# Kernel optimization log

Hardware: AMD Instinct MI355X
Metric: run time of the kernel (lower is better)

The kernel has to match this reference:

```python
import math
import jax, jax.numpy as jnp
import numpy as np

DIM = 1024
NUM_HEADS = 16
HEAD_DIM = DIM // NUM_HEADS


def setup_inputs() -> dict:
    key = jax.random.key(0)
    ks = jax.random.split(key, 5)
    b, t, d = 2, 2048, DIM
    x = jax.random.normal(ks[0], (b, t, d), dtype=jnp.float32)
    mask = jnp.ones((b, t), dtype=jnp.float32)  # 1 = keep, 0 = pad
    s_in = 1.0 / math.sqrt(d)
    w_qkv = jax.random.normal(ks[1], (3 * d, d), dtype=jnp.float32) * s_in
    b_qkv = jnp.zeros((3 * d,), dtype=jnp.float32)
    w_out = jax.random.normal(ks[2], (d, d), dtype=jnp.float32) * s_in
    b_out = jnp.zeros((d,), dtype=jnp.float32)
    return {"x": x, "mask": mask, "w_qkv": w_qkv, "b_qkv": b_qkv,
            "w_out": w_out, "b_out": b_out}


def reference(x, mask, w_qkv, b_qkv, w_out, b_out):
    b, t, d = x.shape
    h, hd = NUM_HEADS, HEAD_DIM
    # qkv projection (torch Linear: x @ W^T + b)
    qkv = x @ w_qkv.T + b_qkv                          # [b,t,3d]
    q, k, v = jnp.split(qkv, 3, axis=-1)
    def reshape(z):
        return z.reshape(b, t, h, hd).transpose(0, 2, 1, 3)  # [b,h,t,hd]
    q, k, v = reshape(q), reshape(k), reshape(v)
    att = jnp.einsum('bhqd,bhkd->bhqk', q, k) / math.sqrt(hd)  # [b,h,t,t]
    causal = jnp.tril(jnp.ones((t, t), dtype=bool))            # [t,t]
    keep = causal[None, None, :, :] & (mask[:, None, None, :] != 0)
    att = jnp.where(keep, att, -jnp.inf)
    att = jax.nn.softmax(att, axis=-1)
    out = jnp.einsum('bhqk,bhkd->bhqd', att, v)        # [b,h,t,hd]
    out = out.transpose(0, 2, 1, 3).reshape(b, t, d)
    return out @ w_out.T + b_out
```

## Files before the change

kernel.cpp:

```cpp
#include <hip/hip_runtime.h>
#include <cmath>

#define B_ 2
#define T_ 2048
#define D_ 1024
#define H_ 16
#define HD_ 64
#define M_ (B_ * T_)
#define N3_ (3 * D_)
#define K_ 1024

typedef _Float16 halfx8 __attribute__((ext_vector_type(8)));
typedef _Float16 halfx4 __attribute__((ext_vector_type(4)));
typedef _Float16 halfx2 __attribute__((ext_vector_type(2)));
typedef __fp16 fp16x2 __attribute__((ext_vector_type(2)));
typedef float f32x4 __attribute__((ext_vector_type(4)));
typedef float f32x16 __attribute__((ext_vector_type(16)));

#define ASYNC_COPY16(gp, lp) \
  __builtin_amdgcn_global_load_lds((__attribute__((address_space(1))) void*)(gp), \
      (__attribute__((address_space(3))) void*)(lp), 16, 0, 0)

#define QSCALE 0.1803368801111204f
#define RTHR 4.0f

__device__ __forceinline__ float exp2fast(float x) {
#if __has_builtin(__builtin_amdgcn_exp2f)
    return __builtin_amdgcn_exp2f(x);
#else
    return exp2f(x);
#endif
}

__device__ const int QT_OF[72] = {
    15,15,15,15,15,15,15,15, 14,14,14,14,14,14,14,14,
    13,13,13,13,13,13,13, 12,12,12,12,12,12,12,
    11,11,11,11,11,11, 10,10,10,10,10,10,
    9,9,9,9,9, 8,8,8,8,8, 7,7,7,7, 6,6,6,6,
    5,5,5, 4,4,4, 3,3, 2,2, 1, 0};
__device__ const int C_OF[72] = {
    0,1,2,3,4,5,6,7, 0,1,2,3,4,5,6,7,
    0,1,2,3,4,5,6, 0,1,2,3,4,5,6,
    0,1,2,3,4,5, 0,1,2,3,4,5,
    0,1,2,3,4, 0,1,2,3,4, 0,1,2,3, 0,1,2,3,
    0,1,2, 0,1,2, 0,1, 0,1, 0, 0};
__device__ const int CB_OF[16] = {0,1,2,4,6,9,12,16,20,25,30,36,42,49,56,64};
__device__ const int NC_OF[16] = {1,1,2,2,3,3,4,4,5,5,6,6,7,7,8,8};
#define NSLOT 72
#define NPOSLOT 56

__global__ __launch_bounds__(256) void prep_all(
    const float* __restrict__ x, const float* __restrict__ wq,
    const float* __restrict__ wo, const float* __restrict__ mask,
    _Float16* __restrict__ xh, _Float16* __restrict__ wqh,
    _Float16* __restrict__ woh, float* __restrict__ kbias,
    int* __restrict__ tflags)
{
    int bid = blockIdx.x;
    if (bid >= 4096) {
        int i = (bid - 4096) * 256 + threadIdx.x;
        float mv = mask[i];
        kbias[i] = (mv != 0.f) ? 0.f : -INFINITY;
        unsigned long long bal = __ballot(mv != 0.f);
        if ((threadIdx.x & 63) == 0) tflags[i >> 6] = (bal == ~0ULL) ? 1 : 0;
        return;
    }
    const float* s; _Float16* d; int off;
    if (bid < 2048)      { s = x;  d = xh;  off = bid; }
    else if (bid < 3584) { s = wq; d = wqh; off = bid - 2048; }
    else                 { s = wo; d = woh; off = bid - 3584; }
    int i = (off * 256 + threadIdx.x) * 8;
    float4 a = *(const float4*)(s + i);
    float4 b = *(const float4*)(s + i + 4);
    halfx8 h;
    h[0] = (_Float16)a.x; h[1] = (_Float16)a.y; h[2] = (_Float16)a.z; h[3] = (_Float16)a.w;
    h[4] = (_Float16)b.x; h[5] = (_Float16)b.y; h[6] = (_Float16)b.z; h[7] = (_Float16)b.w;
    *(halfx8*)(d + i) = h;
}

__global__ __launch_bounds__(256) void gemm_qkv(
    const _Float16* __restrict__ A, const _Float16* __restrict__ Wt,
    const float* __restrict__ bias,
    _Float16* __restrict__ qh, _Float16* __restrict__ kh, _Float16* __restrict__ vth)
{
    __shared__ _Float16 As[128 * 32];
    __shared__ _Float16 Bs[128 * 32];
    const int tid = threadIdx.x;
    const int lane = tid & 63, w = tid >> 6;
    const int col = lane & 15, quad = lane >> 4;
    const int wr = w >> 1, wc = w & 1;
    const int m0 = blockIdx.y << 7, n0 = blockIdx.x << 7;

    const int c0 = w * 2, c1 = c0 + 1;
    const int r0 = c0 * 16 + (lane >> 2), r1 = c1 * 16 + (lane >> 2);
    const int ks = (lane & 3) << 3;

    f32x4 acc[4][4] = {};

    for (int k0 = 0; k0 < K_; k0 += 32) {
        ASYNC_COPY16(A  + (size_t)(m0 + r0) * K_ + k0 + ks, &As[c0 * 512]);
        ASYNC_COPY16(A  + (size_t)(m0 + r1) * K_ + k0 + ks, &As[c1 * 512]);
        ASYNC_COPY16(Wt + (size_t)(n0 + r0) * K_ + k0 + ks, &Bs[c0 * 512]);
        ASYNC_COPY16(Wt + (size_t)(n0 + r1) * K_ + k0 + ks, &Bs[c1 * 512]);
        __syncthreads();
        halfx8 af[4], bf[4];
#pragma unroll
        for (int i = 0; i < 4; ++i)
            af[i] = *(const halfx8*)&As[(wr * 64 + i * 16 + col) * 32 + quad * 8];
#pragma unroll
        for (int j = 0; j < 4; ++j)
            bf[j] = *(const halfx8*)&Bs[(wc * 64 + j * 16 + col) * 32 + quad * 8];
#pragma unroll
        for (int i = 0; i < 4; ++i)
#pragma unroll
            for (int j = 0; j < 4; ++j)
                acc[i][j] = __builtin_amdgcn_mfma_f32_16x16x32_f16(af[i], bf[j], acc[i][j], 0, 0, 0);
        __syncthreads();
    }

#pragma unroll
    for (int i = 0; i < 4; ++i) {
#pragma unroll
        for (int r = 0; r < 4; ++r) {
            int m = m0 + wr * 64 + i * 16 + quad * 4 + r;
            int bb = m >> 11, tt = m & (T_ - 1);
#pragma unroll
            for (int j = 0; j < 4; ++j) {
                int n = n0 + wc * 64 + j * 16 + col;
                float val = acc[i][j][r] + bias[n];
                int which = n >> 10, head = (n >> 6) & 15, dd = n & 63;
                if (which == 0) {
                    qh[((size_t)(bb * H_ + head) * T_ + tt) * HD_ + dd] = (_Float16)(val * QSCALE);
                } else if (which == 1) {
                    int hi = ((dd >> 3) ^ (tt & 7) ^ ((tt >> 3) & 7)) & 7;
                    int dds = (hi << 3) | (dd & 7);
                    kh[((size_t)(bb * H_ + head) * T_ + tt) * HD_ + dds] = (_Float16)val;
                } else {
                    int hi = (((tt >> 3) & 7) ^ (dd & 7) ^ ((dd >> 3) & 7)) & 7;
                    int tts = (tt & ~63) | (hi << 3) | (tt & 7);
                    vth[((size_t)(bb * H_ + head) * HD_ + dd) * T_ + tts] = (_Float16)val;
                }
            }
        }
    }
}

__global__ __launch_bounds__(256) void gemm_out(
    const _Float16* __restrict__ A, const _Float16* __restrict__ Wt,
    const float* __restrict__ bias, float* __restrict__ C)
{
    __shared__ _Float16 As[128 * 32];
    __shared__ _Float16 Bs[64 * 32];
    const int tid = threadIdx.x;
    const int lane = tid & 63, w = tid >> 6;
    const int col = lane & 15, quad = lane >> 4;
    const int m0 = blockIdx.y << 7, n0 = blockIdx.x << 6;

    const int c0 = w * 2, c1 = c0 + 1;
    const int rA0 = c0 * 16 + (lane >> 2), rA1 = c1 * 16 + (lane >> 2);
    const int rB = w * 16 + (lane >> 2);
    const int ks = (lane & 3) << 3;

    f32x4 acc[2][4] = {};

    for (int k0 = 0; k0 < K_; k0 += 32) {
        ASYNC_COPY16(A  + (size_t)(m0 + rA0) * K_ + k0 + ks, &As[c0 * 512]);
        ASYNC_COPY16(A  + (size_t)(m0 + rA1) * K_ + k0 + ks, &As[c1 * 512]);
        ASYNC_COPY16(Wt + (size_t)(n0 + rB) * K_ + k0 + ks, &Bs[w * 512]);
        __syncthreads();
        halfx8 af[2], bf[4];
#pragma unroll
        for (int i = 0; i < 2; ++i)
            af[i] = *(const halfx8*)&As[(w * 32 + i * 16 + col) * 32 + quad * 8];
#pragma unroll
        for (int j = 0; j < 4; ++j)
            bf[j] = *(const halfx8*)&Bs[(j * 16 + col) * 32 + quad * 8];
#pragma unroll
        for (int i = 0; i < 2; ++i)
#pragma unroll
            for (int j = 0; j < 4; ++j)
                acc[i][j] = __builtin_amdgcn_mfma_f32_16x16x32_f16(af[i], bf[j], acc[i][j], 0, 0, 0);
        __syncthreads();
    }

#pragma unroll
    for (int i = 0; i < 2; ++i) {
#pragma unroll
        for (int r = 0; r < 4; ++r) {
            int m = m0 + w * 32 + i * 16 + quad * 4 + r;
#pragma unroll
            for (int j = 0; j < 4; ++j) {
                int n = n0 + j * 16 + col;
                C[(size_t)m * D_ + n] = acc[i][j][r] + bias[n];
            }
        }
    }
}

__global__ __launch_bounds__(256, 3) void attn_kernel(
    const _Float16* __restrict__ qh, const _Float16* __restrict__ kh,
    const _Float16* __restrict__ vth, const float* __restrict__ kbias,
    const int* __restrict__ tflags,
    float* __restrict__ pm, float* __restrict__ pl,
    _Float16* __restrict__ po, _Float16* __restrict__ oh)
{
    __shared__ _Float16 Ks[2][64 * 64];
    __shared__ _Float16 Vt[2][64 * 64];

    const int xi = blockIdx.x;
    const int qt = QT_OF[xi], c = C_OF[xi];
    const int h = blockIdx.y, b = blockIdx.z;
    const int tid = threadIdx.x;
    const int lane = tid & 63, w = tid >> 6;
    const int l31 = lane & 31, q2 = lane >> 5;

    const int kt0 = c * 4;
    const int ktend = min(2 * qt + 1, kt0 + 3);

    const int bh = b * H_ + h;
    const _Float16* qp = qh + (size_t)bh * T_ * HD_;
    const _Float16* kp = kh + (size_t)bh * T_ * HD_;
    const _Float16* vp = vth + (size_t)bh * HD_ * T_;
    const float* kb = kbias + (size_t)b * T_;
    const int* tf = tflags + b * 32;

    const int qbase = qt * 128 + w * 32;
    const int q_row = qbase + l31;

    halfx8 bq[4];
#pragma unroll
    for (int hc = 0; hc < 4; ++hc)
        bq[hc] = *(const halfx8*)(qp + (size_t)q_row * HD_ + hc * 16 + q2 * 8);

    float mrow = -INFINITY;
    float lrow = 0.f;
    f32x16 oacc[2] = {};
    const fp16x2 one2 = {(__fp16)1.f, (__fp16)1.f};

    {
        const _Float16* ksrc = kp + (size_t)(kt0 * 64 + w * 16) * HD_;
        ASYNC_COPY16(ksrc + lane * 8, &Ks[0][(w * 16) * 64]);
        ASYNC_COPY16(ksrc + 8 * HD_ + lane * 8, &Ks[0][(w * 16 + 8) * 64]);
        const _Float16* vsrc = vp + (size_t)(w * 16 + (lane >> 3)) * T_
                                 + kt0 * 64 + (lane & 7) * 8;
        ASYNC_COPY16(vsrc, &Vt[0][(w * 16) * 64]);
        ASYNC_COPY16(vsrc + 8 * T_, &Vt[0][(w * 16 + 8) * 64]);
    }

    for (int kt = kt0; kt <= ktend; ++kt) {
        const int cur = (kt - kt0) & 1;
        __syncthreads();
        if (kt < ktend) {
            const int nb = cur ^ 1;
            const _Float16* ksrc = kp + (size_t)((kt + 1) * 64 + w * 16) * HD_;
            ASYNC_COPY16(ksrc + lane * 8, &Ks[nb][(w * 16) * 64]);
            ASYNC_COPY16(ksrc + 8 * HD_ + lane * 8, &Ks[nb][(w * 16 + 8) * 64]);
            const _Float16* vsrc = vp + (size_t)(w * 16 + (lane >> 3)) * T_
                                     + (kt + 1) * 64 + (lane & 7) * 8;
            ASYNC_COPY16(vsrc, &Vt[nb][(w * 16) * 64]);
            ASYNC_COPY16(vsrc + 8 * T_, &Vt[nb][(w * 16 + 8) * 64]);
        }
        if (kt * 64 > qbase + 31) continue;

        const int allkeep = tf[kt];
        const int kb2max = (qbase + 31 - kt * 64 >= 32) ? 2 : 1;

        auto qk_half = [&](int kb2v) -> f32x16 {
            f32x16 a = {};
#pragma unroll
            for (int hc = 0; hc < 4; ++hc) {
                int seg = (hc * 2 + q2) ^ (l31 & 7) ^ ((kb2v * 4 + (l31 >> 3)) & 7);
                halfx8 ka = *(const halfx8*)&Ks[cur][(kb2v * 32 + l31) * 64 + seg * 8];
                a = __builtin_amdgcn_mfma_f32_32x32x16_f16(ka, bq[hc], a, 0, 0, 0);
            }
            return a;
        };
        f32x16 sa0, sa1;
        __builtin_amdgcn_s_setprio(1);
        sa0 = qk_half(0);
        if (kb2max == 2) sa1 = qk_half(1);
        __builtin_amdgcn_s_setprio(0);

        auto smpv = [&](const f32x16& a, int kb2v) {
            float t0 = fmaxf(fmaxf(a[0],  a[1]),  a[2]);
            float t1 = fmaxf(fmaxf(a[3],  a[4]),  a[5]);
            float t2 = fmaxf(fmaxf(a[6],  a[7]),  a[8]);
            float t3 = fmaxf(fmaxf(a[9],  a[10]), a[11]);
            float t4 = fmaxf(fmaxf(a[12], a[13]), a[14]);
            float u0 = fmaxf(fmaxf(t0, t1), t2);
            float u1 = fmaxf(fmaxf(t3, t4), a[15]);
            float mx = fmaxf(u0, u1);

            if (__any(mx > mrow + RTHR)) {
                float mxo = fmaxf(mx, __shfl_xor(mx, 32, 64));
                float mnew = fmaxf(mrow, mxo);
                float alpha = exp2fast(mrow - mnew);
                lrow *= alpha;
#pragma unroll
                for (int db = 0; db < 2; ++db)
#pragma unroll
                    for (int r = 0; r < 16; ++r) oacc[db][r] *= alpha;
                mrow = mnew;
            }

            const bool fastk = allkeep && (kt * 64 + kb2v * 32 + 31 <= qbase);
            halfx4 pf[4];
            float s0 = 0.f, s1 = 0.f;
            if (fastk) {
#pragma unroll
                for (int cc = 0; cc < 4; ++cc) {
                    float e0 = exp2fast(a[cc * 4 + 0] - mrow);
                    float e1 = exp2fast(a[cc * 4 + 1] - mrow);
                    float e2 = exp2fast(a[cc * 4 + 2] - mrow);
                    float e3 = exp2fast(a[cc * 4 + 3] - mrow);
                    fp16x2 lo = __builtin_amdgcn_cvt_pkrtz(e0, e1);
                    fp16x2 hi = __builtin_amdgcn_cvt_pkrtz(e2, e3);
                    halfx2* pfv = (halfx2*)&pf[cc];
                    pfv[0] = __builtin_bit_cast(halfx2, lo);
                    pfv[1] = __builtin_bit_cast(halfx2, hi);
#if __has_builtin(__builtin_amdgcn_fdot2)
                    s0 = __builtin_amdgcn_fdot2(lo, one2, s0, false);
                    s1 = __builtin_amdgcn_fdot2(hi, one2, s1, false);
#else
                    s0 += e0 + e1; s1 += e2 + e3;
#endif
                }
            } else {
#pragma unroll
                for (int cc = 0; cc < 4; ++cc) {
                    float e[4];
#pragma unroll
                    for (int j = 0; j < 4; ++j) {
                        int key = kt * 64 + kb2v * 32 + 8 * cc + 4 * q2 + j;
                        float add = allkeep ? 0.f : kb[key];
                        e[j] = (key <= q_row) ? exp2fast(a[cc * 4 + j] + add - mrow) : 0.f;
                    }
                    fp16x2 lo = __builtin_amdgcn_cvt_pkrtz(e[0], e[1]);
                    fp16x2 hi = __builtin_amdgcn_cvt_pkrtz(e[2], e[3]);
                    halfx2* pfv = (halfx2*)&pf[cc];
                    pfv[0] = __builtin_bit_cast(halfx2, lo);
                    pfv[1] = __builtin_bit_cast(halfx2, hi);
#if __has_builtin(__builtin_amdgcn_fdot2)
                    s0 = __builtin_amdgcn_fdot2(lo, one2, s0, false);
                    s1 = __builtin_amdgcn_fdot2(hi, one2, s1, false);
#else
                    s0 += e[0] + e[1]; s1 += e[2] + e[3];
#endif
                }
            }
            lrow += s0 + s1;

            __builtin_amdgcn_s_setprio(1);
#pragma unroll
            for (int db = 0; db < 2; ++db)
#pragma unroll
                for (int cc = 0; cc < 4; ++cc) {
                    int ck = kb2v * 4 + cc;
                    int seg = ck ^ (l31 & 7) ^ ((db * 4 + (l31 >> 3)) & 7);
                    halfx4 va = *(const halfx4*)&Vt[cur][(db * 32 + l31) * 64 + seg * 8 + q2 * 4];
                    oacc[db] = __builtin_amdgcn_mfma_f32_32x32x8f16(va, pf[cc], oacc[db], 0, 0, 0);
                }
            __builtin_amdgcn_s_setprio(0);
        };

        smpv(sa0, 0);
        if (kb2max == 2) smpv(sa1, 1);
    }

    lrow += __shfl_xor(lrow, 32, 64);

    const int qloc = w * 32 + l31;
    const int slot = bh * NSLOT + CB_OF[qt] + c;
    if (q2 == 0) {
        pm[(size_t)slot * 128 + qloc] = mrow;
        pl[(size_t)slot * 128 + qloc] = lrow;
    }
    _Float16* pob;
    if (c == 0)
        pob = oh + ((size_t)(b * T_ + qt * 128 + qloc)) * D_ + h * 64;
    else
        pob = po + ((size_t)(bh * NPOSLOT + (CB_OF[qt] - qt) + (c - 1)) * 128 + qloc) * 64;
#pragma unroll
    for (int db = 0; db < 2; ++db)
#pragma unroll
        for (int gg = 0; gg < 4; ++gg) {
            halfx4 ov;
#pragma unroll
            for (int j = 0; j < 4; ++j)
                ov[j] = (_Float16)(oacc[db][gg * 4 + j]);
            *(halfx4*)(pob + db * 32 + 8 * gg + 4 * q2) = ov;
        }
}

__global__ __launch_bounds__(256) void attn_combine(
    const float* __restrict__ pm, const float* __restrict__ pl,
    const _Float16* __restrict__ po, _Float16* __restrict__ oh)
{
    const int qt = blockIdx.x, h = blockIdx.y, b = blockIdx.z;
    const int nc = NC_OF[qt], cb = CB_OF[qt];
    const int bh = b * H_ + h;
    const int tid = threadIdx.x;
    const int r = tid >> 1, dh = tid & 1;

    const int slot0 = bh * NSLOT + cb;
    float mc[8], lc[8];
    float mstar = -INFINITY;
    for (int cc = 0; cc < nc; ++cc) {
        mc[cc] = pm[(size_t)(slot0 + cc) * 128 + r];
        lc[cc] = pl[(size_t)(slot0 + cc) * 128 + r];
        mstar = fmaxf(mstar, mc[cc]);
    }
    float lstar = 0.f, wc[8];
    for (int cc = 0; cc < nc; ++cc) {
        wc[cc] = exp2f(mc[cc] - mstar);
        lstar += wc[cc] * lc[cc];
    }

    _Float16* ohrow = oh + ((size_t)(b * T_ + qt * 128 + r)) * D_ + h * 64 + dh * 32;

    float acc[32];
    {
        float wv = wc[0];
#pragma unroll
        for (int g = 0; g < 4; ++g) {
            halfx8 hv = *(const halfx8*)(ohrow + g * 8);
#pragma unroll
            for (int j = 0; j < 8; ++j)
                acc[g * 8 + j] = wv * (float)hv[j];
        }
    }
    const int pbase = bh * NPOSLOT + (cb - qt);
    for (int cc = 1; cc < nc; ++cc) {
        const _Float16* src = po + ((size_t)(pbase + cc - 1) * 128 + r) * 64 + dh * 32;
        float wv = wc[cc];
#pragma unroll
        for (int g = 0; g < 4; ++g) {
            halfx8 hv = *(const halfx8*)(src + g * 8);
#pragma unroll
            for (int j = 0; j < 8; ++j)
                acc[g * 8 + j] += wv * (float)hv[j];
        }
    }
    float linv = 1.f / lstar;
#pragma unroll
    for (int g = 0; g < 4; ++g) {
        halfx8 ov;
#pragma unroll
        for (int j = 0; j < 8; ++j)
            ov[j] = (_Float16)(acc[g * 8 + j] * linv);
        *(halfx8*)(ohrow + g * 8) = ov;
    }
}

extern "C" void kernel_launch(void* const* d_in, const int* in_sizes, int n_in,
                              void* d_out, int out_size, void* d_ws, size_t ws_size,
                              hipStream_t stream)
{
    (void)in_sizes; (void)n_in; (void)out_size; (void)ws_size;
    const float* x     = (const float*)d_in[0];
    const float* mask  = (const float*)d_in[1];
    const float* w_qkv = (const float*)d_in[2];
    const float* b_qkv = (const float*)d_in[3];
    const float* w_out = (const float*)d_in[4];
    const float* b_out = (const float*)d_in[5];
    float* out = (float*)d_out;

    const size_t QKV1 = (size_t)B_ * H_ * T_ * HD_;
    _Float16* xh  = (_Float16*)d_ws;
    _Float16* wqh = xh  + (size_t)M_ * K_;
    _Float16* woh = wqh + (size_t)N3_ * K_;
    _Float16* qh  = woh + (size_t)D_ * K_;
    _Float16* kh  = qh  + QKV1;
    _Float16* vth = kh  + QKV1;
    _Float16* oh  = vth + QKV1;
    _Float16* po  = oh  + QKV1;
    float* kbias  = (float*)(po + (size_t)32 * NPOSLOT * 128 * 64);
    float* pm     = kbias + (size_t)B_ * T_;
    float* pl     = pm + (size_t)32 * NSLOT * 128;
    int* tflags   = (int*)(pl + (size_t)32 * NSLOT * 128);

    prep_all<<<4112, 256, 0, stream>>>(x, w_qkv, w_out, mask,
                                       xh, wqh, woh, kbias, tflags);
    gemm_qkv<<<dim3(N3_ / 128, M_ / 128), 256, 0, stream>>>(
        xh, wqh, b_qkv, qh, kh, vth);
    attn_kernel<<<dim3(72, H_, B_), 256, 0, stream>>>(
        qh, kh, vth, kbias, tflags, pm, pl, po, oh);
    attn_combine<<<dim3(16, H_, B_), 256, 0, stream>>>(
        pm, pl, po, oh);
    gemm_out<<<dim3(D_ / 64, M_ / 128), 256, 0, stream>>>(
        oh, woh, b_out, out);
}
```

Measured before the change: 196.8 us.

## Drop split-K attention chunks and combine kernel; one block per query tile

Attention blocks now each process a full 128-row query tile against all causal key tiles, launched as a flat 512-block grid ordered from longest to shortest. The partial max/sum/output buffers and the separate combine kernel are removed, and normalization by the row sum happens in the epilogue. This removes a launch and partial-result memory traffic, but it reduces the number of blocks and lengthens the critical path of the largest query tiles, which risks underfilling the GPU.

```diff
diff --git a/kernel.cpp b/kernel.cpp
--- a/kernel.cpp
+++ b/kernel.cpp
@@ -31,23 +31,6 @@
     return exp2f(x);
 #endif
 }
-
-__device__ const int QT_OF[72] = {
-    15,15,15,15,15,15,15,15, 14,14,14,14,14,14,14,14,
-    13,13,13,13,13,13,13, 12,12,12,12,12,12,12,
-    11,11,11,11,11,11, 10,10,10,10,10,10,
-    9,9,9,9,9, 8,8,8,8,8, 7,7,7,7, 6,6,6,6,
-    5,5,5, 4,4,4, 3,3, 2,2, 1, 0};
-__device__ const int C_OF[72] = {
-    0,1,2,3,4,5,6,7, 0,1,2,3,4,5,6,7,
-    0,1,2,3,4,5,6, 0,1,2,3,4,5,6,
-    0,1,2,3,4,5, 0,1,2,3,4,5,
-    0,1,2,3,4, 0,1,2,3,4, 0,1,2,3, 0,1,2,3,
-    0,1,2, 0,1,2, 0,1, 0,1, 0, 0};
-__device__ const int CB_OF[16] = {0,1,2,4,6,9,12,16,20,25,30,36,42,49,56,64};
-__device__ const int NC_OF[16] = {1,1,2,2,3,3,4,4,5,5,6,6,7,7,8,8};
-#define NSLOT 72
-#define NPOSLOT 56
 
 __global__ __launch_bounds__(256) void prep_all(
     const float* __restrict__ x, const float* __restrict__ wq,
@@ -201,21 +184,21 @@
     const _Float16* __restrict__ qh, const _Float16* __restrict__ kh,
     const _Float16* __restrict__ vth, const float* __restrict__ kbias,
     const int* __restrict__ tflags,
-    float* __restrict__ pm, float* __restrict__ pl,
-    _Float16* __restrict__ po, _Float16* __restrict__ oh)
+    _Float16* __restrict__ oh)
 {
     __shared__ _Float16 Ks[2][64 * 64];
     __shared__ _Float16 Vt[2][64 * 64];
 
-    const int xi = blockIdx.x;
-    const int qt = QT_OF[xi], c = C_OF[xi];
-    const int h = blockIdx.y, b = blockIdx.z;
+    const int bid = blockIdx.x;
+    const int qt = 15 - (bid >> 5);
+    const int hb = bid & 31;
+    const int h = hb & 15, b = hb >> 4;
     const int tid = threadIdx.x;
     const int lane = tid & 63, w = tid >> 6;
     const int l31 = lane & 31, q2 = lane >> 5;
 
-    const int kt0 = c * 4;
-    const int ktend = min(2 * qt + 1, kt0 + 3);
+    const int kt0 = 0;
+    const int ktend = 2 * qt + 1;
 
     const int bh = b * H_ + h;
     const _Float16* qp = qh + (size_t)bh * T_ * HD_;
@@ -368,18 +351,10 @@
     }
 
     lrow += __shfl_xor(lrow, 32, 64);
+    const float linv = 1.f / lrow;
 
     const int qloc = w * 32 + l31;
-    const int slot = bh * NSLOT + CB_OF[qt] + c;
-    if (q2 == 0) {
-        pm[(size_t)slot * 128 + qloc] = mrow;
-        pl[(size_t)slot * 128 + qloc] = lrow;
-    }
-    _Float16* pob;
-    if (c == 0)
-        pob = oh + ((size_t)(b * T_ + qt * 128 + qloc)) * D_ + h * 64;
-    else
-        pob = po + ((size_t)(bh * NPOSLOT + (CB_OF[qt] - qt) + (c - 1)) * 128 + qloc) * 64;
+    _Float16* pob = oh + ((size_t)(b * T_ + qt * 128 + qloc)) * D_ + h * 64;
 #pragma unroll
     for (int db = 0; db < 2; ++db)
 #pragma unroll
@@ -387,69 +362,9 @@
             halfx4 ov;
 #pragma unroll
             for (int j = 0; j < 4; ++j)
-                ov[j] = (_Float16)(oacc[db][gg * 4 + j]);
+                ov[j] = (_Float16)(oacc[db][gg * 4 + j] * linv);
             *(halfx4*)(pob + db * 32 + 8 * gg + 4 * q2) = ov;
         }
-}
-
-__global__ __launch_bounds__(256) void attn_combine(
-    const float* __restrict__ pm, const float* __restrict__ pl,
-    const _Float16* __restrict__ po, _Float16* __restrict__ oh)
-{
-    const int qt = blockIdx.x, h = blockIdx.y, b = blockIdx.z;
-    const int nc = NC_OF[qt], cb = CB_OF[qt];
-    const int bh = b * H_ + h;
-    const int tid = threadIdx.x;
-    const int r = tid >> 1, dh = tid & 1;
-
-    const int slot0 = bh * NSLOT + cb;
-    float mc[8], lc[8];
-    float mstar = -INFINITY;
-    for (int cc = 0; cc < nc; ++cc) {
-        mc[cc] = pm[(size_t)(slot0 + cc) * 128 + r];
-        lc[cc] = pl[(size_t)(slot0 + cc) * 128 + r];
-        mstar = fmaxf(mstar, mc[cc]);
-    }
-    float lstar = 0.f, wc[8];
-    for (int cc = 0; cc < nc; ++cc) {
-        wc[cc] = exp2f(mc[cc] - mstar);
-        lstar += wc[cc] * lc[cc];
-    }
-
-    _Float16* ohrow = oh + ((size_t)(b * T_ + qt * 128 + r)) * D_ + h * 64 + dh * 32;
-
-    float acc[32];
-    {
-        float wv = wc[0];
-#pragma unroll
-        for (int g = 0; g < 4; ++g) {
-            halfx8 hv = *(const halfx8*)(ohrow + g * 8);
-#pragma unroll
-            for (int j = 0; j < 8; ++j)
-                acc[g * 8 + j] = wv * (float)hv[j];
-        }
-    }
-    const int pbase = bh * NPOSLOT + (cb - qt);
-    for (int cc = 1; cc < nc; ++cc) {
-        const _Float16* src = po + ((size_t)(pbase + cc - 1) * 128 + r) * 64 + dh * 32;
-        float wv = wc[cc];
-#pragma unroll
-        for (int g = 0; g < 4; ++g) {
-            halfx8 hv = *(const halfx8*)(src + g * 8);
-#pragma unroll
-            for (int j = 0; j < 8; ++j)
-                acc[g * 8 + j] += wv * (float)hv[j];
-        }
-    }
-    float linv = 1.f / lstar;
-#pragma unroll
-    for (int g = 0; g < 4; ++g) {
-        halfx8 ov;
-#pragma unroll
-        for (int j = 0; j < 8; ++j)
-            ov[j] = (_Float16)(acc[g * 8 + j] * linv);
-        *(halfx8*)(ohrow + g * 8) = ov;
-    }
 }
 
 extern "C" void kernel_launch(void* const* d_in, const int* in_sizes, int n_in,
@@ -473,20 +388,15 @@
     _Float16* kh  = qh  + QKV1;
     _Float16* vth = kh  + QKV1;
     _Float16* oh  = vth + QKV1;
-    _Float16* po  = oh  + QKV1;
-    float* kbias  = (float*)(po + (size_t)32 * NPOSLOT * 128 * 64);
-    float* pm     = kbias + (size_t)B_ * T_;
-    float* pl     = pm + (size_t)32 * NSLOT * 128;
-    int* tflags   = (int*)(pl + (size_t)32 * NSLOT * 128);
+    float* kbias  = (float*)(oh + QKV1);
+    int* tflags   = (int*)(kbias + (size_t)B_ * T_);
 
     prep_all<<<4112, 256, 0, stream>>>(x, w_qkv, w_out, mask,
                                        xh, wqh, woh, kbias, tflags);
     gemm_qkv<<<dim3(N3_ / 128, M_ / 128), 256, 0, stream>>>(
         xh, wqh, b_qkv, qh, kh, vth);
-    attn_kernel<<<dim3(72, H_, B_), 256, 0, stream>>>(
-        qh, kh, vth, kbias, tflags, pm, pl, po, oh);
-    attn_combine<<<dim3(16, H_, B_), 256, 0, stream>>>(
-        pm, pl, po, oh);
+    attn_kernel<<<dim3(512, 1, 1), 256, 0, stream>>>(
+        qh, kh, vth, kbias, tflags, oh);
     gemm_out<<<dim3(D_ / 64, M_ / 128), 256, 0, stream>>>(
         oh, woh, b_out, out);
 }
```

New measurement: 193.4 us. Within noise of the previous version (-1.7%).
